# Optimization experiments

Hardware: AMD Instinct MI355X
Metric: run time of the kernel (lower is better)

## Reference

```python
import jax, jax.numpy as jnp
import numpy as np

NP, NT, H, FT, E, EL = 200000, 100000, 64, 64, 2000000, 500000


def _seg_mean(msg, dst, n):
    s = jax.ops.segment_sum(msg, dst, num_segments=n)
    c = jax.ops.segment_sum(jnp.ones(dst.shape, msg.dtype), dst, num_segments=n)
    return s / jnp.maximum(c, 1.0)[:, None]


def _sage(x_src, x_dst, src, dst, wl, bl, wr):
    # PyG SAGEConv (aggr='mean'): lin_l(mean_neighbors) + lin_r(x_dst); lin_r has no bias
    mean = _seg_mean(x_src[src], dst, x_dst.shape[0])
    return mean @ wl + bl + x_dst @ wr


def setup_inputs() -> dict:
    key = jax.random.key(0)
    ks = jax.random.split(key, 24)
    s = 1.0 / np.sqrt(H)
    inp = {
        "x_taxon": jax.random.normal(ks[0], (NT, FT), jnp.float32),
        "taxon_lin_w": jax.random.normal(ks[1], (FT, H), jnp.float32) * (1.0 / np.sqrt(FT)),
        "taxon_lin_b": jax.random.normal(ks[2], (H,), jnp.float32) * 0.01,
        "palmprint_emb": jax.random.normal(ks[3], (NP, H), jnp.float32),
        "taxon_emb": jax.random.normal(ks[4], (NT, H), jnp.float32),
        "n_id_palmprint": jnp.arange(NP, dtype=jnp.int64),
        "n_id_taxon": jnp.arange(NT, dtype=jnp.int64),
        "edge_src": jax.random.randint(ks[5], (E,), 0, NP, jnp.int64),
        "edge_dst": jax.random.randint(ks[6], (E,), 0, NT, jnp.int64),
        "el_src": jax.random.randint(ks[7], (EL,), 0, NP, jnp.int64),
        "el_dst": jax.random.randint(ks[8], (EL,), 0, NT, jnp.int64),
    }
    names = ["c1pt_wl", "c1pt_wr", "c1tp_wl", "c1tp_wr", "c2pt_wl", "c2pt_wr", "c2tp_wl", "c2tp_wr"]
    for i, nm in enumerate(names):
        inp[nm] = jax.random.normal(ks[9 + i], (H, H), jnp.float32) * s
    for i, nm in enumerate(["c1pt_bl", "c1tp_bl", "c2pt_bl", "c2tp_bl"]):
        inp[nm] = jax.random.normal(ks[17 + i], (H,), jnp.float32) * 0.01
    return inp


def reference(x_taxon, taxon_lin_w, taxon_lin_b, palmprint_emb, taxon_emb,
              c1pt_wl, c1pt_wr, c1tp_wl, c1tp_wr, c2pt_wl, c2pt_wr, c2tp_wl, c2tp_wr,
              c1pt_bl, c1tp_bl, c2pt_bl, c2tp_bl,
              n_id_palmprint, n_id_taxon, edge_src, edge_dst, el_src, el_dst):
    # initial features (use_embeddings=True)
    x_p = palmprint_emb[n_id_palmprint]                       # [NP, H]
    x_t = x_taxon @ taxon_lin_w + taxon_lin_b + taxon_emb[n_id_taxon]  # [NT, H]

    # layer 1: p->t and t->p (reverse edges), then ReLU
    t1 = _sage(x_p, x_t, edge_src, edge_dst, c1pt_wl, c1pt_bl, c1pt_wr)
    p1 = _sage(x_t, x_p, edge_dst, edge_src, c1tp_wl, c1tp_bl, c1tp_wr)
    p1, t1 = jax.nn.relu(p1), jax.nn.relu(t1)

    # layer 2
    t2 = _sage(p1, t1, edge_src, edge_dst, c2pt_wl, c2pt_bl, c2pt_wr)
    p2 = _sage(t1, p1, edge_dst, edge_src, c2tp_wl, c2tp_bl, c2tp_wr)

    # classifier: per-supervision-edge dot product
    return jnp.sum(p2[el_src] * t2[el_dst], axis=-1)          # [EL]
```

## Files before the change

kernel.cpp:

```cpp
#include <hip/hip_runtime.h>

#define H 64
#define EPB 4096
#define BMAX 400
#define ST 256
#define SP 512
#define LSHT 18
#define LSHP 17
#define CAPB 5632

typedef _Float16 half2v __attribute__((ext_vector_type(2)));
typedef _Float16 half8v __attribute__((ext_vector_type(8)));
typedef _Float16 f16x8  __attribute__((ext_vector_type(8)));
typedef float    f32x4  __attribute__((ext_vector_type(4)));
typedef int      i32x4  __attribute__((ext_vector_type(4)));

#if defined(__has_builtin)
#if __has_builtin(__builtin_amdgcn_fdot2)
#define HAS_FDOT2 1
#endif
#endif

#define MFMA16(a, b, c) __builtin_amdgcn_mfma_f32_16x16x32_f16(a, b, c, 0, 0, 0)

template <int HALF_IN>
__device__ __forceinline__ void mfma_dual_dev(const void* __restrict__ Av,
                                              const float* __restrict__ W1,
                                              const float* __restrict__ W2,
                                              const float* __restrict__ b2,
                                              _Float16* __restrict__ C1,
                                              _Float16* __restrict__ C2,
                                              int N, int wid, int nwaves) {
    const int lane = threadIdx.x & 63;
    const int m = lane & 15, quad = lane >> 4;
    const int nTiles = (N + 15) >> 4;

    f16x8 w1f[2][4], w2f[2][4];
#pragma unroll
    for (int kh = 0; kh < 2; ++kh)
#pragma unroll
        for (int nt = 0; nt < 4; ++nt) {
            f16x8 a, b;
#pragma unroll
            for (int j = 0; j < 8; ++j) {
                int k = kh * 32 + quad * 8 + j;
                a[j] = (_Float16)W1[k * 64 + nt * 16 + m];
                b[j] = (_Float16)W2[k * 64 + nt * 16 + m];
            }
            w1f[kh][nt] = a;
            w2f[kh][nt] = b;
        }
    float bv[4];
#pragma unroll
    for (int nt = 0; nt < 4; ++nt) bv[nt] = b2[nt * 16 + m];

    for (int t = wid; t < nTiles; t += nwaves) {
        int row = t * 16 + m;
        f16x8 alo = {}, ahi = {};
        if (row < N) {
            if (HALF_IN) {
                const f16x8* A8 = (const f16x8*)Av;
                alo = A8[(size_t)row * 8 + quad];
                ahi = A8[(size_t)row * 8 + 4 + quad];
            } else {
                const float4* p = (const float4*)((const float*)Av + (size_t)row * 64);
                float4 x0 = p[quad * 2], x1 = p[quad * 2 + 1];
                float4 x2 = p[8 + quad * 2], x3 = p[8 + quad * 2 + 1];
                alo[0] = (_Float16)x0.x; alo[1] = (_Float16)x0.y;
                alo[2] = (_Float16)x0.z; alo[3] = (_Float16)x0.w;
                alo[4] = (_Float16)x1.x; alo[5] = (_Float16)x1.y;
                alo[6] = (_Float16)x1.z; alo[7] = (_Float16)x1.w;
                ahi[0] = (_Float16)x2.x; ahi[1] = (_Float16)x2.y;
                ahi[2] = (_Float16)x2.z; ahi[3] = (_Float16)x2.w;
                ahi[4] = (_Float16)x3.x; ahi[5] = (_Float16)x3.y;
                ahi[6] = (_Float16)x3.z; ahi[7] = (_Float16)x3.w;
            }
        }
#pragma unroll
        for (int nt = 0; nt < 4; ++nt) {
            f32x4 a1 = {0.f, 0.f, 0.f, 0.f}, a2 = {0.f, 0.f, 0.f, 0.f};
            a1 = MFMA16(alo, w1f[0][nt], a1);
            a1 = MFMA16(ahi, w1f[1][nt], a1);
            a2 = MFMA16(alo, w2f[0][nt], a2);
            a2 = MFMA16(ahi, w2f[1][nt], a2);
#pragma unroll
            for (int r = 0; r < 4; ++r) {
                int orow = t * 16 + quad * 4 + r;
                if (orow < N) {
                    C1[(size_t)orow * 64 + nt * 16 + m] = (_Float16)a1[r];
                    C2[(size_t)orow * 64 + nt * 16 + m] = (_Float16)(a2[r] + bv[nt]);
                }
            }
        }
    }
}

__device__ __forceinline__ void mfma_xt_dev(const float* __restrict__ A,
                                            const float* __restrict__ W,
                                            const float* __restrict__ bias,
                                            const float* __restrict__ addend,
                                            _Float16* __restrict__ C,
                                            int N, int wid, int nwaves) {
    const int lane = threadIdx.x & 63;
    const int m = lane & 15, quad = lane >> 4;
    const int nTiles = (N + 15) >> 4;

    f16x8 wf[2][4];
#pragma unroll
    for (int kh = 0; kh < 2; ++kh)
#pragma unroll
        for (int nt = 0; nt < 4; ++nt) {
            f16x8 a;
#pragma unroll
            for (int j = 0; j < 8; ++j) {
                int k = kh * 32 + quad * 8 + j;
                a[j] = (_Float16)W[k * 64 + nt * 16 + m];
            }
            wf[kh][nt] = a;
        }
    float bv[4];
#pragma unroll
    for (int nt = 0; nt < 4; ++nt) bv[nt] = bias[nt * 16 + m];

    for (int t = wid; t < nTiles; t += nwaves) {
        int row = t * 16 + m;
        f16x8 alo = {}, ahi = {};
        if (row < N) {
            const float4* p = (const float4*)(A + (size_t)row * 64);
            float4 x0 = p[quad * 2], x1 = p[quad * 2 + 1];
            float4 x2 = p[8 + quad * 2], x3 = p[8 + quad * 2 + 1];
            alo[0] = (_Float16)x0.x; alo[1] = (_Float16)x0.y;
            alo[2] = (_Float16)x0.z; alo[3] = (_Float16)x0.w;
            alo[4] = (_Float16)x1.x; alo[5] = (_Float16)x1.y;
            alo[6] = (_Float16)x1.z; alo[7] = (_Float16)x1.w;
            ahi[0] = (_Float16)x2.x; ahi[1] = (_Float16)x2.y;
            ahi[2] = (_Float16)x2.z; ahi[3] = (_Float16)x2.w;
            ahi[4] = (_Float16)x3.x; ahi[5] = (_Float16)x3.y;
            ahi[6] = (_Float16)x3.z; ahi[7] = (_Float16)x3.w;
        }
#pragma unroll
        for (int nt = 0; nt < 4; ++nt) {
            f32x4 a1 = {0.f, 0.f, 0.f, 0.f};
            a1 = MFMA16(alo, wf[0][nt], a1);
            a1 = MFMA16(ahi, wf[1][nt], a1);
#pragma unroll
            for (int r = 0; r < 4; ++r) {
                int orow = t * 16 + quad * 4 + r;
                if (orow < N) {
                    float ad = addend[(size_t)orow * 64 + nt * 16 + m];
                    C[(size_t)orow * 64 + nt * 16 + m] = (_Float16)(a1[r] + bv[nt] + ad);
                }
            }
        }
    }
}

__global__ void __launch_bounds__(256) k_bin_xt(
    const int* __restrict__ src, const int* __restrict__ dst,
    int* __restrict__ curT, int* __restrict__ curP,
    unsigned* __restrict__ binT, unsigned* __restrict__ binP,
    int BT, int BP, int E, int nbBin,
    const float* __restrict__ A, const float* __restrict__ W,
    const float* __restrict__ bias, const float* __restrict__ addend,
    _Float16* __restrict__ C, int NT_, int xtBlocks) {
    __shared__ int cT[BMAX], cP[BMAX], oT[BMAX], oP[BMAX];
    int tid = threadIdx.x;
    if ((int)blockIdx.x >= nbBin) {
        int xb = blockIdx.x - nbBin;
        mfma_xt_dev(A, W, bias, addend, C, NT_, xb * 4 + (tid >> 6), xtBlocks * 4);
        return;
    }
    for (int i = tid; i < BMAX; i += 256) { cT[i] = 0; cP[i] = 0; }
    __syncthreads();
    int e0 = blockIdx.x * EPB;
    int ls[EPB / 256], ld[EPB / 256];
#pragma unroll
    for (int k = 0; k < EPB / 256; ++k) {
        int i = e0 + k * 256 + tid;
        if (i < E) {
            ls[k] = src[i];
            ld[k] = dst[i];
            atomicAdd(&cT[ld[k] >> 8], 1);
            atomicAdd(&cP[ls[k] >> 9], 1);
        }
    }
    __syncthreads();
    for (int b = tid; b < BT; b += 256) { int c = cT[b]; oT[b] = c ? atomicAdd(&curT[b], c) : 0; cT[b] = 0; }
    for (int b = tid; b < BP; b += 256) { int c = cP[b]; oP[b] = c ? atomicAdd(&curP[b], c) : 0; cP[b] = 0; }
    __syncthreads();
#pragma unroll
    for (int k = 0; k < EPB / 256; ++k) {
        int i = e0 + k * 256 + tid;
        if (i < E) {
            int s = ls[k], d = ld[k];
            int bt = d >> 8, bp = s >> 9;
            int rt = oT[bt] + atomicAdd(&cT[bt], 1);
            int rp = oP[bp] + atomicAdd(&cP[bp], 1);
            if (rt < CAPB) binT[(size_t)bt * CAPB + rt] = ((unsigned)(d & 255) << LSHT) | (unsigned)s;
            if (rp < CAPB) binP[(size_t)bp * CAPB + rp] = ((unsigned)(s & 511) << LSHP) | (unsigned)d;
        }
    }
}

__device__ __forceinline__ void csr_dev(const unsigned* __restrict__ binned,
                                        const int* __restrict__ cur,
                                        int* __restrict__ start_g, int* __restrict__ cnt_g,
                                        int* __restrict__ adj,
                                        int S, int lshift, int N, int b,
                                        int* lcnt, int* lscan, int* lcur, int* adj_lds) {
    int tid = threadIdx.x;
    int base = b * CAPB;
    int n = cur[b]; if (n > CAPB) n = CAPB;
    int rowlo = b * S;
    unsigned nbmask = (1u << lshift) - 1u;

    for (int i = tid; i < S; i += 256) lcnt[i] = 0;
    __syncthreads();
    for (int i = tid; i < n; i += 256)
        atomicAdd(&lcnt[binned[base + i] >> lshift], 1);
    __syncthreads();
    for (int i = tid; i < S; i += 256) lscan[i] = lcnt[i];
    __syncthreads();
    for (int off = 1; off < S; off <<= 1) {
        int i0 = tid, i1 = tid + 256;
        int v0 = (i0 >= off) ? lscan[i0 - off] : 0;
        int v1 = (S > 256 && i1 >= off) ? lscan[i1 - off] : 0;
        __syncthreads();
        if (i0 < S) lscan[i0] += v0;
        if (S > 256 && i1 < S) lscan[i1] += v1;
        __syncthreads();
    }
    for (int r = tid; r < S; r += 256) {
        int ex = lscan[r] - lcnt[r];
        lcur[r] = ex;
        int row = rowlo + r;
        if (row < N) {
            start_g[row] = base + ex;
            cnt_g[row]   = lcnt[r];
        }
    }
    __syncthreads();
    for (int i = tid; i < n; i += 256) {
        unsigned e = binned[base + i];
        int r = e >> lshift;
        int pos = atomicAdd(&lcur[r], 1);
        adj_lds[pos] = (int)(e & nbmask);
    }
    __syncthreads();
    int n4 = n & ~3;
    for (int i = tid * 4; i < n4; i += 1024)
        *(int4*)&adj[base + i] = *(const int4*)&adj_lds[i];
    for (int i = n4 + tid; i < n; i += 256)
        adj[base + i] = adj_lds[i];
}

__global__ void __launch_bounds__(256) k_csr_mfma1(
    const unsigned* __restrict__ binT, const unsigned* __restrict__ binP,
    const int* __restrict__ curT, const int* __restrict__ curP,
    int* __restrict__ start_t, int* __restrict__ cnt_t, int* __restrict__ adj_t,
    int* __restrict__ start_p, int* __restrict__ cnt_p, int* __restrict__ adj_p,
    int BT, int BP, int NT_, int NP_,
    const _Float16* __restrict__ XTh, const float* __restrict__ Wt1, const float* __restrict__ Wt2,
    const float* __restrict__ bt2, _Float16* __restrict__ Aht, _Float16* __restrict__ Bth,
    const float* __restrict__ pemb, const float* __restrict__ Wp1, const float* __restrict__ Wp2,
    const float* __restrict__ bp2, _Float16* __restrict__ Ahp, _Float16* __restrict__ Bph,
    int tB, int pB) {
    __shared__ int lcnt[512], lscan[512], lcur[512];
    __shared__ int adj_lds[CAPB];
    int bi = blockIdx.x;
    if (bi < BT) {
        csr_dev(binT, curT, start_t, cnt_t, adj_t, ST, LSHT, NT_, bi, lcnt, lscan, lcur, adj_lds);
    } else if (bi < BT + BP) {
        csr_dev(binP, curP, start_p, cnt_p, adj_p, SP, LSHP, NP_, bi - BT, lcnt, lscan, lcur, adj_lds);
    } else if (bi < BT + BP + tB) {
        int wb = bi - BT - BP;
        mfma_dual_dev<1>(XTh, Wt1, Wt2, bt2, Aht, Bth, NT_, wb * 4 + (threadIdx.x >> 6), tB * 4);
    } else {
        int wb = bi - BT - BP - tB;
        mfma_dual_dev<0>(pemb, Wp1, Wp2, bp2, Ahp, Bph, NP_, wb * 4 + (threadIdx.x >> 6), pB * 4);
    }
}

__global__ void __launch_bounds__(256) k_mfma2(
    const _Float16* __restrict__ T1h, const float* __restrict__ Wt1, const float* __restrict__ Wt2,
    const float* __restrict__ bt2, _Float16* __restrict__ Aht, _Float16* __restrict__ Bth,
    const _Float16* __restrict__ P1h, const float* __restrict__ Wp1, const float* __restrict__ Wp2,
    const float* __restrict__ bp2, _Float16* __restrict__ Ahp, _Float16* __restrict__ Bph,
    int NT_, int NP_, int tB, int pB) {
    int bi = blockIdx.x;
    if (bi < tB)
        mfma_dual_dev<1>(T1h, Wt1, Wt2, bt2, Aht, Bth, NT_, bi * 4 + (threadIdx.x >> 6), tB * 4);
    else
        mfma_dual_dev<1>(P1h, Wp1, Wp2, bp2, Ahp, Bph, NP_, (bi - tB) * 4 + (threadIdx.x >> 6), pB * 4);
}

__device__ __forceinline__ void gather_dev(
    const int* __restrict__ adj, const int* __restrict__ start, const int* __restrict__ cnt,
    const _Float16* __restrict__ A, const _Float16* __restrict__ B,
    _Float16* __restrict__ out, int do_relu, int N, int gidx) {
    int row = gidx >> 3;
    int c   = gidx & 7;
    if (row >= N) return;

    int st = start[row], dg = cnt[row];
    const half8v* A8 = (const half8v*)A;
    half8v acc = {};
    int j = 0;
    for (; j + 3 < dg; j += 4) {
        int n0 = adj[st + j], n1 = adj[st + j + 1];
        int n2 = adj[st + j + 2], n3 = adj[st + j + 3];
        half8v v0 = A8[(size_t)n0 * 8 + c];
        half8v v1 = A8[(size_t)n1 * 8 + c];
        half8v v2 = A8[(size_t)n2 * 8 + c];
        half8v v3 = A8[(size_t)n3 * 8 + c];
        acc += (v0 + v1) + (v2 + v3);
    }
    for (; j < dg; ++j) acc += A8[(size_t)adj[st + j] * 8 + c];

    float inv = 1.0f / (float)(dg > 1 ? dg : 1);
    half8v b8 = ((const half8v*)B)[(size_t)row * 8 + c];
    half8v o;
#pragma unroll
    for (int k = 0; k < 8; ++k) {
        float v = (float)acc[k] * inv + (float)b8[k];
        if (do_relu) v = fmaxf(v, 0.f);
        o[k] = (_Float16)v;
    }
    i32x4 oi;
    __builtin_memcpy(&oi, &o, sizeof(oi));
    __builtin_nontemporal_store(oi, (i32x4*)&((half8v*)out)[(size_t)row * 8 + c]);
}

__global__ void __launch_bounds__(256) k_gather2(
    const int* __restrict__ adjT, const int* __restrict__ startT, const int* __restrict__ cntT,
    const _Float16* __restrict__ At, const _Float16* __restrict__ Bt, _Float16* __restrict__ outT, int NT_,
    const int* __restrict__ adjP, const int* __restrict__ startP, const int* __restrict__ cntP,
    const _Float16* __restrict__ Ap, const _Float16* __restrict__ Bp, _Float16* __restrict__ outP, int NP_,
    int do_relu, int wTb) {
    if ((int)blockIdx.x < wTb)
        gather_dev(adjT, startT, cntT, At, Bt, outT, do_relu, NT_, blockIdx.x * 256 + threadIdx.x);
    else
        gather_dev(adjP, startP, cntP, Ap, Bp, outP, do_relu, NP_,
                   (blockIdx.x - wTb) * 256 + threadIdx.x);
}

__global__ void __launch_bounds__(256) dot_h(const _Float16* __restrict__ p2,
                                             const _Float16* __restrict__ t2,
                                             const int* __restrict__ els,
                                             const int* __restrict__ eld,
                                             float* __restrict__ out, int EL) {
    int tid = blockIdx.x * 256 + threadIdx.x;
    int i = tid >> 3, c = tid & 7;
    if (i < EL) {
        int s = els[i], d = eld[i];
        half8v a = ((const half8v*)p2)[(size_t)s * 8 + c];
        half8v b = ((const half8v*)t2)[(size_t)d * 8 + c];
        float v = 0.f;
#ifdef HAS_FDOT2
        const half2v* ap = (const half2v*)&a;
        const half2v* bp = (const half2v*)&b;
#pragma unroll
        for (int k = 0; k < 4; ++k) v = __builtin_amdgcn_fdot2(ap[k], bp[k], v, false);
#else
#pragma unroll
        for (int k = 0; k < 8; ++k) v += (float)a[k] * (float)b[k];
#endif
        v += __shfl_xor(v, 1, 64);
        v += __shfl_xor(v, 2, 64);
        v += __shfl_xor(v, 4, 64);
        if (c == 0) out[i] = v;
    }
}

extern "C" void kernel_launch(void* const* d_in, const int* in_sizes, int n_in,
                              void* d_out, int out_size, void* d_ws, size_t ws_size,
                              hipStream_t stream) {
    const float* x_taxon  = (const float*)d_in[0];
    const float* tlw      = (const float*)d_in[1];
    const float* tlb      = (const float*)d_in[2];
    const float* pemb     = (const float*)d_in[3];
    const float* temb     = (const float*)d_in[4];
    const int*   edge_src = (const int*)d_in[7];
    const int*   edge_dst = (const int*)d_in[8];
    const int*   el_src   = (const int*)d_in[9];
    const int*   el_dst   = (const int*)d_in[10];
    const float* c1pt_wl  = (const float*)d_in[11];
    const float* c1pt_wr  = (const float*)d_in[12];
    const float* c1tp_wl  = (const float*)d_in[13];
    const float* c1tp_wr  = (const float*)d_in[14];
    const float* c2pt_wl  = (const float*)d_in[15];
    const float* c2pt_wr  = (const float*)d_in[16];
    const float* c2tp_wl  = (const float*)d_in[17];
    const float* c2tp_wr  = (const float*)d_in[18];
    const float* c1pt_bl  = (const float*)d_in[19];
    const float* c1tp_bl  = (const float*)d_in[20];
    const float* c2pt_bl  = (const float*)d_in[21];
    const float* c2tp_bl  = (const float*)d_in[22];

    const int NP_ = in_sizes[5];
    const int NT_ = in_sizes[6];
    const int E_  = in_sizes[7];
    const int EL_ = in_sizes[9];
    const int BT  = (NT_ + ST - 1) / ST;
    const int BP  = (NP_ + SP - 1) / SP;

    _Float16* hb  = (_Float16*)d_ws;
    _Float16* XTh = hb;
    _Float16* T1h = XTh + (size_t)NT_ * H;
    _Float16* P1h = T1h + (size_t)NT_ * H;
    _Float16* Aht = P1h + (size_t)NP_ * H;
    _Float16* Ahp = Aht + (size_t)NT_ * H;
    _Float16* Bth = Ahp + (size_t)NP_ * H;
    _Float16* Bph = Bth + (size_t)NT_ * H;
    _Float16* P2h = Bph + (size_t)NP_ * H;
    _Float16* T2h = XTh;

    unsigned* binT    = (unsigned*)(P2h + (size_t)NP_ * H);
    unsigned* binP    = binT + (size_t)BT * CAPB;
    int*      adj_t   = (int*)(binP + (size_t)BP * CAPB);
    int*      adj_p   = adj_t + (size_t)BT * CAPB;
    int* start_t = adj_p + (size_t)BP * CAPB;
    int* start_p = start_t + NT_;
    int* cnt_t   = start_p + NP_;
    int* cnt_p   = cnt_t + NT_;
    int* curT    = cnt_p + NP_;
    int* curP    = curT + BMAX;

    (void)hipMemsetAsync(curT, 0, 2 * BMAX * sizeof(int), stream);

    const int nbBin = (E_ + EPB - 1) / EPB;
    const int XTB   = 512;
    const int wT = (NT_ * 8 + 255) / 256, wP = (NP_ * 8 + 255) / 256;
    const int tB = 256, pB = 512;

    k_bin_xt<<<nbBin + XTB, 256, 0, stream>>>(
        edge_src, edge_dst, curT, curP, binT, binP, BT, BP, E_, nbBin,
        x_taxon, tlw, tlb, temb, XTh, NT_, XTB);

    k_csr_mfma1<<<BT + BP + tB + pB, 256, 0, stream>>>(
        binT, binP, curT, curP,
        start_t, cnt_t, adj_t, start_p, cnt_p, adj_p, BT, BP, NT_, NP_,
        XTh, c1tp_wl, c1pt_wr, c1pt_bl, Aht, Bth,
        pemb, c1pt_wl, c1tp_wr, c1tp_bl, Ahp, Bph, tB, pB);

    k_gather2<<<wT + wP, 256, 0, stream>>>(
        adj_t, start_t, cnt_t, Ahp, Bth, T1h, NT_,
        adj_p, start_p, cnt_p, Aht, Bph, P1h, NP_, 1, wT);

    k_mfma2<<<tB + pB, 256, 0, stream>>>(
        T1h, c2tp_wl, c2pt_wr, c2pt_bl, Aht, Bth,
        P1h, c2pt_wl, c2tp_wr, c2tp_bl, Ahp, Bph, NT_, NP_, tB, pB);

    k_gather2<<<wT + wP, 256, 0, stream>>>(
        adj_t, start_t, cnt_t, Ahp, Bth, T2h, NT_,
        adj_p, start_p, cnt_p, Aht, Bph, P2h, NP_, 0, wT);

    dot_h<<<(EL_ * 8 + 255) / 256, 256, 0, stream>>>(P2h, T2h, el_src, el_dst,
                                                     (float*)d_out, EL_);
}
```

Measured before the change: 479.2 us.

## Stage binned edges in LDS for coalesced writes; unroll gather by eight

The binning kernel now counting-sorts each block's edges by bucket in shared memory, using a block-wide prefix scan, before writing them out. One wave then writes each bucket's contiguous run to global memory, so the scattered per-edge global stores become coalesced ones. The neighbour gather loop is unrolled from four to eight loads per iteration to keep more memory requests in flight. In exchange the binning kernel uses extra LDS (a 16 KB stage buffer), runs two scans with many barriers, and may see lower occupancy.

```diff
diff --git a/kernel.cpp b/kernel.cpp
--- a/kernel.cpp
+++ b/kernel.cpp
@@ -155,6 +155,18 @@
     }
 }
 
+__device__ __forceinline__ void block_scan512(int* sc, int tid) {
+    for (int off = 1; off < 512; off <<= 1) {
+        int i0 = tid, i1 = tid + 256;
+        int v0 = (i0 >= off) ? sc[i0 - off] : 0;
+        int v1 = (i1 >= off) ? sc[i1 - off] : 0;
+        __syncthreads();
+        sc[i0] += v0;
+        sc[i1] += v1;
+        __syncthreads();
+    }
+}
+
 __global__ void __launch_bounds__(256) k_bin_xt(
     const int* __restrict__ src, const int* __restrict__ dst,
     int* __restrict__ curT, int* __restrict__ curP,
@@ -163,13 +175,16 @@
     const float* __restrict__ A, const float* __restrict__ W,
     const float* __restrict__ bias, const float* __restrict__ addend,
     _Float16* __restrict__ C, int NT_, int xtBlocks) {
-    __shared__ int cT[BMAX], cP[BMAX], oT[BMAX], oP[BMAX];
+    __shared__ int cT[BMAX], cP[BMAX], oT[BMAX], oP[BMAX], cur[BMAX];
+    __shared__ int sc[512];
+    __shared__ unsigned stage[EPB];
     int tid = threadIdx.x;
     if ((int)blockIdx.x >= nbBin) {
         int xb = blockIdx.x - nbBin;
         mfma_xt_dev(A, W, bias, addend, C, NT_, xb * 4 + (tid >> 6), xtBlocks * 4);
         return;
     }
+    const int wave = tid >> 6, lane = tid & 63;
     for (int i = tid; i < BMAX; i += 256) { cT[i] = 0; cP[i] = 0; }
     __syncthreads();
     int e0 = blockIdx.x * EPB;
@@ -185,19 +200,53 @@
         }
     }
     __syncthreads();
-    for (int b = tid; b < BT; b += 256) { int c = cT[b]; oT[b] = c ? atomicAdd(&curT[b], c) : 0; cT[b] = 0; }
-    for (int b = tid; b < BP; b += 256) { int c = cP[b]; oP[b] = c ? atomicAdd(&curP[b], c) : 0; cP[b] = 0; }
+    for (int b = tid; b < BT; b += 256) { int c = cT[b]; oT[b] = c ? atomicAdd(&curT[b], c) : 0; }
+    for (int b = tid; b < BP; b += 256) { int c = cP[b]; oP[b] = c ? atomicAdd(&curP[b], c) : 0; }
+    sc[tid]       = (tid < BT) ? cT[tid] : 0;
+    sc[tid + 256] = (tid + 256 < BT) ? cT[tid + 256] : 0;
+    __syncthreads();
+    block_scan512(sc, tid);
+    for (int b = tid; b < BT; b += 256) cur[b] = sc[b] - cT[b];
     __syncthreads();
 #pragma unroll
     for (int k = 0; k < EPB / 256; ++k) {
         int i = e0 + k * 256 + tid;
         if (i < E) {
-            int s = ls[k], d = ld[k];
-            int bt = d >> 8, bp = s >> 9;
-            int rt = oT[bt] + atomicAdd(&cT[bt], 1);
-            int rp = oP[bp] + atomicAdd(&cP[bp], 1);
-            if (rt < CAPB) binT[(size_t)bt * CAPB + rt] = ((unsigned)(d & 255) << LSHT) | (unsigned)s;
-            if (rp < CAPB) binP[(size_t)bp * CAPB + rp] = ((unsigned)(s & 511) << LSHP) | (unsigned)d;
+            int bt = ld[k] >> 8;
+            int pos = atomicAdd(&cur[bt], 1);
+            stage[pos] = ((unsigned)(ld[k] & 255) << LSHT) | (unsigned)ls[k];
+        }
+    }
+    __syncthreads();
+    for (int b = wave; b < BT; b += 4) {
+        int cnt = cT[b], so = sc[b] - cnt, go = oT[b];
+        for (int i = lane; i < cnt; i += 64) {
+            int pos = go + i;
+            if (pos < CAPB) binT[(size_t)b * CAPB + pos] = stage[so + i];
+        }
+    }
+    __syncthreads();
+    sc[tid]       = (tid < BP) ? cP[tid] : 0;
+    sc[tid + 256] = (tid + 256 < BP) ? cP[tid + 256] : 0;
+    __syncthreads();
+    block_scan512(sc, tid);
+    for (int b = tid; b < BP; b += 256) cur[b] = sc[b] - cP[b];
+    __syncthreads();
+#pragma unroll
+    for (int k = 0; k < EPB / 256; ++k) {
+        int i = e0 + k * 256 + tid;
+        if (i < E) {
+            int bp = ls[k] >> 9;
+            int pos = atomicAdd(&cur[bp], 1);
+            stage[pos] = ((unsigned)(ls[k] & 511) << LSHP) | (unsigned)ld[k];
+        }
+    }
+    __syncthreads();
+    for (int b = wave; b < BP; b += 4) {
+        int cnt = cP[b], so = sc[b] - cnt, go = oP[b];
+        for (int i = lane; i < cnt; i += 64) {
+            int pos = go + i;
+            if (pos < CAPB) binP[(size_t)b * CAPB + pos] = stage[so + i];
         }
     }
 }
@@ -306,14 +355,30 @@
     const half8v* A8 = (const half8v*)A;
     half8v acc = {};
     int j = 0;
-    for (; j + 3 < dg; j += 4) {
-        int n0 = adj[st + j], n1 = adj[st + j + 1];
+    for (; j + 7 < dg; j += 8) {
+        int n0 = adj[st + j],     n1 = adj[st + j + 1];
+        int n2 = adj[st + j + 2], n3 = adj[st + j + 3];
+        int n4 = adj[st + j + 4], n5 = adj[st + j + 5];
+        int n6 = adj[st + j + 6], n7 = adj[st + j + 7];
+        half8v v0 = A8[(size_t)n0 * 8 + c];
+        half8v v1 = A8[(size_t)n1 * 8 + c];
+        half8v v2 = A8[(size_t)n2 * 8 + c];
+        half8v v3 = A8[(size_t)n3 * 8 + c];
+        half8v v4 = A8[(size_t)n4 * 8 + c];
+        half8v v5 = A8[(size_t)n5 * 8 + c];
+        half8v v6 = A8[(size_t)n6 * 8 + c];
+        half8v v7 = A8[(size_t)n7 * 8 + c];
+        acc += ((v0 + v1) + (v2 + v3)) + ((v4 + v5) + (v6 + v7));
+    }
+    if (j + 3 < dg) {
+        int n0 = adj[st + j],     n1 = adj[st + j + 1];
         int n2 = adj[st + j + 2], n3 = adj[st + j + 3];
         half8v v0 = A8[(size_t)n0 * 8 + c];
         half8v v1 = A8[(size_t)n1 * 8 + c];
         half8v v2 = A8[(size_t)n2 * 8 + c];
         half8v v3 = A8[(size_t)n3 * 8 + c];
         acc += (v0 + v1) + (v2 + v3);
+        j += 4;
     }
     for (; j < dg; ++j) acc += A8[(size_t)adj[st + j] * 8 + c];
 
```

Measured after the change: 476.3 us. No clear change (-0.6%).
